# Performance work log

Hardware: AMD Instinct MI355X
Metric: run time of the kernel (lower is better)

## Reference

```python
import jax, jax.numpy as jnp
import numpy as np
from jax import lax

B, A, H, W = 16, 9, 128, 128
STRIDE = 16
MIN_SIZE = 16.0


def _generate_anchors():
    base = 16.0
    ratios = np.array([0.5, 1.0, 2.0])
    scales = np.array([8.0, 16.0, 32.0])
    ctr = (base - 1.0) / 2.0
    size = base * base
    ws0 = np.round(np.sqrt(size / ratios))
    hs0 = np.round(ws0 * ratios)
    ws = (ws0[:, None] * scales[None, :]).reshape(-1)  # [9]
    hs = (hs0[:, None] * scales[None, :]).reshape(-1)
    base_anchors = np.stack([ctr - 0.5 * (ws - 1), ctr - 0.5 * (hs - 1),
                             ctr + 0.5 * (ws - 1), ctr + 0.5 * (hs - 1)], axis=1)  # [9,4]
    sx = np.arange(W) * STRIDE
    sy = np.arange(H) * STRIDE
    shift_x, shift_y = np.meshgrid(sx, sy)  # [H,W]
    shifts = np.stack([shift_x, shift_y, shift_x, shift_y], axis=-1).reshape(H * W, 1, 4)
    return (shifts + base_anchors[None]).reshape(-1, 4).astype(np.float32)  # [H*W*A,4]


def setup_inputs() -> dict:
    key = jax.random.key(0)
    k1, k2 = jax.random.split(key)
    scores = jax.random.normal(k1, (B, 2 * A, H, W), jnp.float32)
    bbox_deltas = jax.random.normal(k2, (B, 4 * A, H, W), jnp.float32) * 0.1
    anchors = jnp.asarray(_generate_anchors())
    im_info = jnp.tile(jnp.array([H * STRIDE, W * STRIDE, 1.0, 1.0], jnp.float32), (B, 1))
    return {"scores": scores, "bbox_deltas": bbox_deltas, "anchors": anchors,
            "im_info": im_info, "num_anchors": A, "pre_nms": 2000, "post_nms": 300,
            "nms_thresh": 0.7}


def _iou_matrix(b):
    x1, y1, x2, y2 = b[:, 0], b[:, 1], b[:, 2], b[:, 3]
    area = (x2 - x1 + 1.0) * (y2 - y1 + 1.0)
    iw = jnp.maximum(jnp.minimum(x2[:, None], x2[None, :]) - jnp.maximum(x1[:, None], x1[None, :]) + 1.0, 0.0)
    ih = jnp.maximum(jnp.minimum(y2[:, None], y2[None, :]) - jnp.maximum(y1[:, None], y1[None, :]) + 1.0, 0.0)
    inter = iw * ih
    return inter / (area[:, None] + area[None, :] - inter)


def reference(scores, bbox_deltas, anchors, im_info, num_anchors, pre_nms, post_nms, nms_thresh):
    batch = bbox_deltas.shape[0]
    feat_w = scores.shape[3]
    # deltas -> [B, H*W*A, 4]
    deltas = bbox_deltas.transpose(0, 2, 3, 1).reshape(batch, -1, 4)
    # fg/bg softmax exactly as in the module
    s = jax.nn.softmax(scores.reshape(batch, 2, -1, feat_w), axis=1)
    s = s.reshape(batch, num_anchors * 2, -1, feat_w)[:, num_anchors:, :, :]
    s = s.transpose(0, 2, 3, 1).reshape(batch, -1)  # [B, H*W*A]
    anc = jnp.broadcast_to(anchors.reshape(1, -1, 4), deltas.shape)
    # bbox_transform_inv
    widths = anc[..., 2] - anc[..., 0] + 1.0
    heights = anc[..., 3] - anc[..., 1] + 1.0
    ctr_x = anc[..., 0] + 0.5 * widths
    ctr_y = anc[..., 1] + 0.5 * heights
    dx, dy, dw, dh = deltas[..., 0], deltas[..., 1], deltas[..., 2], deltas[..., 3]
    pcx = dx * widths + ctr_x
    pcy = dy * heights + ctr_y
    pw = jnp.exp(dw) * widths
    ph = jnp.exp(dh) * heights
    proposals = jnp.stack([pcx - 0.5 * pw, pcy - 0.5 * ph, pcx + 0.5 * pw, pcy + 0.5 * ph], axis=-1)
    # clip_boxes to image extent (im_info = [h, w, sy, sx])
    w_max = (im_info[:, 1] - 1.0)[:, None]
    h_max = (im_info[:, 0] - 1.0)[:, None]
    proposals = jnp.stack([
        jnp.clip(proposals[..., 0], 0.0, w_max),
        jnp.clip(proposals[..., 1], 0.0, h_max),
        jnp.clip(proposals[..., 2], 0.0, w_max),
        jnp.clip(proposals[..., 3], 0.0, h_max)], axis=-1)

    ar = jnp.arange(pre_nms)

    def per_image(props, scr, info):
        ws = props[:, 2] - props[:, 0] + 1.0
        hs = props[:, 3] - props[:, 1] + 1.0
        valid = (ws >= MIN_SIZE * info[3]) & (hs >= MIN_SIZE * info[2])
        masked = jnp.where(valid, scr, -jnp.inf)
        vals, idx = lax.top_k(masked, pre_nms)  # sort desc + truncate to pre_nms
        boxes = props[idx]  # [pre_nms, 4], score-sorted
        live = jnp.isfinite(vals)  # drop filtered boxes if fewer than pre_nms survive
        iou = _iou_matrix(boxes)  # [pre_nms, pre_nms]
        def body(i, keep):
            sup = keep[i] & (iou[i] > nms_thresh) & (ar > i)
            return keep & (~sup)
        keep = lax.fori_loop(0, pre_nms, body, live)  # greedy NMS over sorted boxes
        pos = jnp.where(keep, jnp.cumsum(keep) - 1, post_nms)
        kept = jnp.zeros((post_nms, 4), boxes.dtype).at[pos].set(boxes, mode='drop')
        return kept

    kept = jax.vmap(per_image)(proposals, s, im_info)  # [B, post_nms, 4]
    bidx = jnp.broadcast_to(jnp.arange(batch, dtype=kept.dtype)[:, None, None], (batch, post_nms, 1))
    output = jnp.concatenate([bidx, kept], axis=-1)  # [B, post_nms, 5]
    return output, proposals
```

## Files before the change

kernel.cpp:

```cpp
#include <hip/hip_runtime.h>
#include <stdint.h>

#define B_ 16
#define A_ 9
#define H_ 128
#define W_ 128
#define HW_ (H_*W_)
#define N_ (HW_*A_)
#define PRE_ 2000
#define POST_ 300
#define CAND_CAP 4096
#define SEG_ 32

typedef unsigned int u32;
typedef unsigned long long u64;

#define OFF_STATE  0ull
#define OFF_HIST0  1024ull
#define OFF_HIST1  (OFF_HIST0 + 16384ull)
#define OFF_KEYS   (OFF_HIST1 + 16384ull)
#define OFF_CAND   (OFF_KEYS + (u64)B_*N_*4)
#define OFF_SELBOX (OFF_CAND + (u64)B_*CAND_CAP*8)
#define OFF_LIVE   (OFF_SELBOX + (u64)B_*PRE_*16)
#define OFF_SUPP   (OFF_LIVE + (u64)B_*32*8)

__device__ __forceinline__ u32 mono_key(float f) {
    u32 u = __float_as_uint(f);
    return (u & 0x80000000u) ? ~u : (u | 0x80000000u);
}

__device__ __forceinline__ u64 shfl64(u64 v, int src) {
    u32 lo = (u32)__shfl((int)(u32)(v & 0xFFFFFFFFull), src);
    u32 hi = (u32)__shfl((int)(u32)(v >> 32), src);
    return ((u64)hi << 32) | lo;
}

__device__ __forceinline__ void wave_select256(const u32* __restrict__ hh, u32 need,
                                               u32* __restrict__ out) {
    int lane = threadIdx.x & 63;
    uint4 hv = ((const uint4*)hh)[lane];
    u32 psum = hv.x + hv.y + hv.z + hv.w;
    u32 s = psum;
    #pragma unroll
    for (int off = 1; off < 64; off <<= 1) {
        u32 o = (u32)__shfl_down((int)s, off);
        if (lane + off < 64) s += o;
    }
    u32 S_next = (u32)__shfl_down((int)s, 1);
    if (lane == 63) S_next = 0;
    u32 above[4], cnt[4];
    above[3] = S_next;             cnt[3] = hv.w;
    above[2] = S_next + hv.w;      cnt[2] = hv.z;
    above[1] = above[2] + hv.z;    cnt[1] = hv.y;
    above[0] = above[1] + hv.y;    cnt[0] = hv.x;
    #pragma unroll
    for (int j = 3; j >= 0; --j) {
        if (above[j] < need && above[j] + cnt[j] >= need) {
            out[0] = (u32)(4*lane + j);
            out[1] = need - above[j];
        }
    }
}

__global__ __launch_bounds__(576) void decode_kernel(
        const float* __restrict__ scores,
        const float* __restrict__ deltas,
        const float* __restrict__ anchors,
        const float* __restrict__ im_info,
        float* __restrict__ outprop,
        u32* __restrict__ keys,
        u32* __restrict__ hist0) {
    __shared__ float4 tile[9][65];
    __shared__ float4 sbase[A_];
    __shared__ u32 h[256];
    int tid = threadIdx.x;
    int a = tid >> 6, lane = tid & 63;
    if (tid < A_) sbase[tid] = ((const float4*)anchors)[tid];
    if (tid < 256) h[tid] = 0;
    __syncthreads();

    int b  = blockIdx.x >> 8;
    int pb = blockIdx.x & 255;
    int p0 = pb << 6;
    int p  = p0 + lane;

    float s0 = scores[((b*2*A_ + a)      << 14) + p];
    float s1 = scores[((b*2*A_ + A_ + a) << 14) + p];
    float m  = fmaxf(s0, s1);
    float e0 = expf(s0 - m);
    float e1 = expf(s1 - m);
    float fg = e1 / (e0 + e1);

    float4 base = sbase[a];
    int ix = p & (W_-1), iy = p >> 7;
    float sx = (float)(ix * 16), sy = (float)(iy * 16);
    float ax1 = base.x + sx, ay1 = base.y + sy, ax2 = base.z + sx, ay2 = base.w + sy;

    float w  = ax2 - ax1 + 1.0f;
    float h_ = ay2 - ay1 + 1.0f;
    float cx = ax1 + 0.5f*w;
    float cy = ay1 + 0.5f*h_;

    const float* dbase = deltas + (u64)(((b*4*A_ + 4*a) << 14) + p);
    float dx = dbase[0];
    float dy = dbase[HW_];
    float dw = dbase[2*HW_];
    float dh = dbase[3*HW_];

    float pcx = dx*w  + cx;
    float pcy = dy*h_ + cy;
    float pw  = expf(dw)*w;
    float ph  = expf(dh)*h_;
    float x1 = pcx - 0.5f*pw, y1 = pcy - 0.5f*ph;
    float x2 = pcx + 0.5f*pw, y2 = pcy + 0.5f*ph;

    float wmax = im_info[b*4 + 1] - 1.0f;
    float hmax = im_info[b*4 + 0] - 1.0f;
    x1 = fminf(fmaxf(x1, 0.0f), wmax);
    y1 = fminf(fmaxf(y1, 0.0f), hmax);
    x2 = fminf(fmaxf(x2, 0.0f), wmax);
    y2 = fminf(fmaxf(y2, 0.0f), hmax);

    tile[a][lane] = make_float4(x1, y1, x2, y2);

    float bw = x2 - x1 + 1.0f;
    float bh = y2 - y1 + 1.0f;
    bool valid = (bw >= 16.0f*im_info[b*4 + 3]) && (bh >= 16.0f*im_info[b*4 + 2]);
    float sc = valid ? fg : -__builtin_inff();
    u32 k = mono_key(sc);
    keys[((u64)(b*A_ + a) << 14) + p] = k;
    atomicAdd(&h[k >> 24], 1u);
    __syncthreads();

    int a2 = tid % 9, pl = tid / 9;
    ((float4*)outprop)[(u64)b*N_ + p0*9 + tid] = tile[a2][pl];

    if (tid < 256 && h[tid]) atomicAdd(&hist0[b*256 + tid], h[tid]);
}

__global__ __launch_bounds__(1024) void hist16_kernel(
        const u32* __restrict__ keys, const u32* __restrict__ hist0,
        u32* __restrict__ hist1) {
    int b = blockIdx.x >> 4;
    int slice = blockIdx.x & 15;
    int tid = threadIdx.x;
    __shared__ u32 sel[2];
    __shared__ u32 h[256];
    if (tid < 64) wave_select256(hist0 + b*256, (u32)PRE_, sel);
    for (int i = tid; i < 256; i += 1024) h[i] = 0;
    __syncthreads();
    u32 pfx = sel[0];
    const u32* kb = keys + (u64)b*N_ + slice*(N_/16);
    for (int n = tid; n < N_/16; n += 1024) {
        u32 k = kb[n];
        if ((k >> 24) == pfx) atomicAdd(&h[(k >> 16) & 255u], 1u);
    }
    __syncthreads();
    for (int i = tid; i < 256; i += 1024)
        if (h[i]) atomicAdd(&hist1[b*256 + i], h[i]);
}

__global__ __launch_bounds__(1024) void collect_kernel(
        const u32* __restrict__ keys, const u32* __restrict__ hist0,
        const u32* __restrict__ hist1, u32* __restrict__ state,
        u64* __restrict__ cand) {
    int b = blockIdx.x >> 4;
    int slice = blockIdx.x & 15;
    int tid = threadIdx.x;
    int wave = tid >> 6, lane = tid & 63;
    __shared__ u32 sel8[2], sel16[2];
    __shared__ u32 wbase[16];
    __shared__ u32 s_base;
    if (tid < 64) wave_select256(hist0 + b*256, (u32)PRE_, sel8);
    __syncthreads();
    if (tid < 64) wave_select256(hist1 + b*256, sel8[1], sel16);
    __syncthreads();
    u32 T = (sel8[0] << 24) | (sel16[0] << 16);

    const u32* kb = keys + (u64)b*N_ + slice*(N_/16);
    u64* cb = cand + (u64)b*CAND_CAP;

    u32 kreg[9];
    int c = 0;
    #pragma unroll
    for (int r = 0; r < 9; ++r) {
        kreg[r] = kb[tid + r*1024];
        c += (kreg[r] >= T) ? 1 : 0;
    }

    int x = c;
    #pragma unroll
    for (int off = 1; off < 64; off <<= 1) {
        int y = __shfl_up(x, off);
        if (lane >= off) x += y;
    }
    if (lane == 63) wbase[wave] = (u32)x;
    __syncthreads();
    if (tid == 0) {
        u32 acc = 0;
        #pragma unroll
        for (int w2 = 0; w2 < 16; ++w2) { u32 t2 = wbase[w2]; wbase[w2] = acc; acc += t2; }
        s_base = acc ? atomicAdd(&state[b*8 + 2], acc) : 0u;
    }
    __syncthreads();

    u32 pos = s_base + wbase[wave] + (u32)(x - c);
    #pragma unroll
    for (int r = 0; r < 9; ++r) {
        if (kreg[r] >= T) {
            int idx = slice*(N_/16) + tid + r*1024;
            u32 n = (u32)((idx & (HW_-1))*A_ + (idx >> 14));
            if (pos < CAND_CAP) cb[pos] = ((u64)kreg[r] << 32) | (u32)(~n);
            pos++;
        }
    }
}

__global__ __launch_bounds__(1024) void rank_kernel(
        const u64* __restrict__ cand, const u32* __restrict__ state,
        const float* __restrict__ outprop,
        float4* __restrict__ selbox, u32* __restrict__ selkey) {
    int bi = blockIdx.x;
    int b = bi >> 4, chunk = bi & 15;
    int tid = threadIdx.x;
    int q = tid >> 8, ti = tid & 255;
    __shared__ __align__(16) u64 sc[CAND_CAP];
    __shared__ u32 prank[256];

    u32 cnt = state[b*8 + 2];
    if (cnt > CAND_CAP) cnt = CAND_CAP;
    const u64* cb = cand + (u64)b*CAND_CAP;
    for (int j = tid; j < CAND_CAP; j += 1024) sc[j] = (j < (int)cnt) ? cb[j] : 0ull;
    if (tid < 256) prank[tid] = 0;
    __syncthreads();

    int i = (chunk << 8) + ti;
    u64 mine = sc[i];

    int pairs = ((int)cnt + 1) >> 1;
    int pq = (pairs + 3) >> 2;
    int p0 = q * pq;
    int p1 = p0 + pq; if (p1 > pairs) p1 = pairs;
    const ulonglong2* sl = (const ulonglong2*)sc;
    u32 c = 0;
    #pragma unroll 8
    for (int p = p0; p < p1; ++p) {
        ulonglong2 v = sl[p];
        c += (v.x > mine) ? 1u : 0u;
        c += (v.y > mine) ? 1u : 0u;
    }
    if (c) atomicAdd(&prank[ti], c);
    __syncthreads();

    if (q == 0 && i < (int)cnt) {
        u32 rank = prank[ti];
        if (rank < PRE_) {
            u32 n = ~(u32)mine;
            float4 box = ((const float4*)outprop)[(u64)b*N_ + n];
            selbox[(u64)b*PRE_ + rank] = box;
            selkey[b*2048 + rank] = (u32)(mine >> 32);
        }
    }
}

__global__ __launch_bounds__(256) void iou_kernel(
        const float4* __restrict__ selbox, const float* __restrict__ thrp,
        u64* __restrict__ supp) {
    int bi = blockIdx.x;
    int b = bi / 250;
    int rbase = (bi % 250) * 8;
    int c0 = rbase >> 8;
    int tid = threadIdx.x;
    __shared__ float4 box[PRE_];
    for (int i = (c0 << 8) + tid; i < PRE_; i += 256) box[i] = selbox[(u64)b*PRE_ + i];
    __syncthreads();
    float thresh = thrp[0];
    int wv = tid >> 6, lane = tid & 63;

    float4 p[8]; float ai[8];
    #pragma unroll
    for (int r = 0; r < 8; ++r) {
        p[r]  = box[rbase + r];
        ai[r] = (p[r].z - p[r].x + 1.f) * (p[r].w - p[r].y + 1.f);
    }
    for (int c = c0; c < 8; ++c) {
        int j = c*256 + tid;
        bool inb = (j < PRE_);
        float4 q = box[inb ? j : 0];
        float aj = (q.z - q.x + 1.f) * (q.w - q.y + 1.f);
        #pragma unroll
        for (int r = 0; r < 8; ++r) {
            float iw = fminf(p[r].z, q.z) - fmaxf(p[r].x, q.x) + 1.f;
            float ih = fminf(p[r].w, q.w) - fmaxf(p[r].y, q.y) + 1.f;
            float inter = fmaxf(iw, 0.f) * ih;
            float su = ai[r] + aj;
            float un = su - inter;
            float m  = __fmaf_rn(-thresh, un, inter);
            bool pred = m > 0.0f;
            if (__any(fabsf(m) <= 2.0f)) {
                pred = (inter / un) > thresh;
            }
            pred = pred && inb;
            u64 ball = __ballot(pred);
            if (lane == 0)
                supp[((u64)(b*PRE_ + rbase + r))*32 + (c*4 + wv)] = ball;
        }
    }
}

__global__ __launch_bounds__(256) void scan_kernel(
        const u64* __restrict__ supp, const u32* __restrict__ selkey,
        const float4* __restrict__ selbox, float* __restrict__ out0) {
    int b = blockIdx.x;
    int tid = threadIdx.x;
    int wave = tid >> 6, lane = tid & 63;

    __shared__ u64 sdiag[SEG_][64];
    __shared__ u64 lwords[32];
    __shared__ u64 keptmask[SEG_];
    __shared__ int kept[POST_];
    __shared__ int s_kc;

    for (int e = tid; e < SEG_*64; e += 256) {
        int g = e >> 6;
        sdiag[g][e & 63] = (e < PRE_) ? supp[((u64)(b*PRE_ + e))*32 + g] : 0ull;
    }
    #pragma unroll
    for (int k = 0; k < 8; ++k) {
        int r = k*256 + tid;
        u32 kk = selkey[b*2048 + r];
        u64 bal = __ballot((r < PRE_) && (kk >= 0x80000000u));
        if (lane == 0) lwords[k*4 + wave] = bal;
    }
    if (tid < SEG_) keptmask[tid] = 0ull;
    if (tid == 0) s_kc = 0;
    __syncthreads();

    if (wave == 0) {
        u64 aliveW = (lane < 32) ? lwords[lane] : 0ull;
        int kc = 0;
        for (int g = 0; g < SEG_ && kc < POST_; ++g) {
            u64 aw = shfl64(aliveW, g);
            if (!aw) continue;
            u64 dj = sdiag[g][lane];
            int base = g << 6;

            u64 a = aw;
            u64 ks = 0;
            while (a && kc < POST_) {
                int i = (int)__builtin_ctzll(a);
                ks |= (1ull << i);
                kc++;
                bool killed = ((dj >> i) & 1ull) != 0ull;
                u64 km = __ballot(killed);
                a &= ~km;
                a &= ~(1ull << i);
            }
            if (lane == 0) keptmask[g] = ks;
            if (kc >= POST_) break;

            bool ld = (lane > g) && (lane < 32);
            u64 t = ks;
            u64 orr = 0ull;
            const u64* rb = supp + ((u64)(b*PRE_ + base))*32 + (lane & 31);
            while (t) {
                int i0 = (int)__builtin_ctzll(t);
                int id[16];
                #pragma unroll
                for (int k = 0; k < 16; ++k) {
                    id[k] = t ? (int)__builtin_ctzll(t) : i0;
                    if (t) t &= t - 1;
                }
                u64 v[16];
                #pragma unroll
                for (int k = 0; k < 16; ++k)
                    v[k] = ld ? rb[(u64)id[k] * 32] : 0ull;
                u64 o = 0ull;
                #pragma unroll
                for (int k = 0; k < 16; ++k) o |= v[k];
                orr |= o;
            }
            aliveW &= ~orr;
        }
        if (lane == 0) s_kc = kc;
    }
    __syncthreads();

    if (wave == 0) {
        u64 w = (lane < 32) ? keptmask[lane] : 0ull;
        int pc = (int)__builtin_popcountll(w);
        int x = pc;
        #pragma unroll
        for (int off = 1; off < 64; off <<= 1) {
            int y = __shfl_up(x, off);
            if (lane >= off) x += y;
        }
        int pr = x - pc;
        u64 t = w;
        int c = 0;
        while (t) {
            int bit = (int)__builtin_ctzll(t);
            t &= t - 1;
            int pos = pr + c; c++;
            if (pos < POST_) kept[pos] = lane*64 + bit;
        }
    }
    __syncthreads();

    int kc = s_kc;
    for (int r = tid; r < POST_; r += 256) {
        int i = (r < kc) ? kept[r] : -1;
        float o1 = 0.f, o2 = 0.f, o3 = 0.f, o4 = 0.f;
        if (i >= 0) {
            float4 bx = selbox[(u64)b*PRE_ + i];
            o1 = bx.x; o2 = bx.y; o3 = bx.z; o4 = bx.w;
        }
        float* rowp = out0 + (u64)(b*POST_ + r)*5;
        rowp[0] = (float)b;
        rowp[1] = o1; rowp[2] = o2; rowp[3] = o3; rowp[4] = o4;
    }
}

extern "C" void kernel_launch(void* const* d_in, const int* in_sizes, int n_in,
                              void* d_out, int out_size, void* d_ws, size_t ws_size,
                              hipStream_t stream) {
    const float* scores  = (const float*)d_in[0];
    const float* deltas  = (const float*)d_in[1];
    const float* anchors = (const float*)d_in[2];
    const float* im_info = (const float*)d_in[3];
    const float* thrp    = (const float*)d_in[7];

    float* out0    = (float*)d_out;
    float* outprop = out0 + (u64)B_*POST_*5;

    char* ws = (char*)d_ws;
    u32*    state  = (u32*)   (ws + OFF_STATE);
    u32*    hist0  = (u32*)   (ws + OFF_HIST0);
    u32*    hist1  = (u32*)   (ws + OFF_HIST1);
    u32*    keys   = (u32*)   (ws + OFF_KEYS);
    u64*    cand   = (u64*)   (ws + OFF_CAND);
    float4* selbox = (float4*)(ws + OFF_SELBOX);
    u64*    supp   = (u64*)   (ws + OFF_SUPP);
    u32*    selkey = (u32*)   (ws + OFF_KEYS);

    hipMemsetAsync(ws, 0, OFF_KEYS, stream);

    decode_kernel<<<B_*256, 576, 0, stream>>>(scores, deltas, anchors, im_info, outprop, keys, hist0);
    hist16_kernel<<<B_*16, 1024, 0, stream>>>(keys, hist0, hist1);
    collect_kernel<<<B_*16, 1024, 0, stream>>>(keys, hist0, hist1, state, cand);
    rank_kernel<<<B_*16, 1024, 0, stream>>>(cand, state, outprop, selbox, selkey);
    iou_kernel<<<B_*250, 256, 0, stream>>>(selbox, thrp, supp);
    scan_kernel<<<B_, 256, 0, stream>>>(supp, selkey, selbox, out0);
}
```

Measured before the change: 227.1 us.

## Double-buffer suppression mask segments in shared memory for the NMS scan

The serial NMS scan no longer has wave 0 gather suppression rows from global memory. All four waves now cooperatively prefetch each 64-row segment of the mask matrix into a padded, double-buffered shared-memory tile, working one segment ahead through registers. Wave 0 then reads both the diagonal word and the kept rows from LDS, taking global latency off the serial critical path. The cost is a block-wide barrier per segment, about 34KB of LDS, and extra register pressure from the prefetch staging.

```diff
diff --git a/kernel.cpp b/kernel.cpp
--- a/kernel.cpp
+++ b/kernel.cpp
@@ -308,23 +308,19 @@
     }
 }
 
-__global__ __launch_bounds__(256) void scan_kernel(
+__global__ __launch_bounds__(256, 1) void scan_kernel(
         const u64* __restrict__ supp, const u32* __restrict__ selkey,
         const float4* __restrict__ selbox, float* __restrict__ out0) {
     int b = blockIdx.x;
     int tid = threadIdx.x;
     int wave = tid >> 6, lane = tid & 63;
 
-    __shared__ u64 sdiag[SEG_][64];
+    __shared__ u64 rbuf[2][64][33];
     __shared__ u64 lwords[32];
     __shared__ u64 keptmask[SEG_];
     __shared__ int kept[POST_];
     __shared__ int s_kc;
 
-    for (int e = tid; e < SEG_*64; e += 256) {
-        int g = e >> 6;
-        sdiag[g][e & 63] = (e < PRE_) ? supp[((u64)(b*PRE_ + e))*32 + g] : 0ull;
-    }
     #pragma unroll
     for (int k = 0; k < 8; ++k) {
         int r = k*256 + tid;
@@ -334,57 +330,90 @@
     }
     if (tid < SEG_) keptmask[tid] = 0ull;
     if (tid == 0) s_kc = 0;
-    __syncthreads();
-
-    if (wave == 0) {
-        u64 aliveW = (lane < 32) ? lwords[lane] : 0ull;
-        int kc = 0;
-        for (int g = 0; g < SEG_ && kc < POST_; ++g) {
+
+    const u64* sb = supp + (u64)b*PRE_*32;
+
+    u64 gr[8];
+    #pragma unroll
+    for (int k = 0; k < 8; ++k) {
+        int f = tid + (k << 8);
+        gr[k] = sb[(u64)(f >> 5)*32 + (f & 31)];
+    }
+    #pragma unroll
+    for (int k = 0; k < 8; ++k) {
+        int f = tid + (k << 8);
+        rbuf[0][f >> 5][f & 31] = gr[k];
+    }
+    #pragma unroll
+    for (int k = 0; k < 8; ++k) {
+        int f = tid + (k << 8);
+        gr[k] = sb[(u64)(64 + (f >> 5))*32 + (f & 31)];
+    }
+    __syncthreads();
+
+    u64 aliveW = 0ull;
+    if (wave == 0 && lane < 32) aliveW = lwords[lane];
+    int kc = 0;
+    int ll = lane & 31;
+
+    for (int g = 0; g < SEG_; ++g) {
+        int cur = g & 1;
+        if (g + 1 < SEG_) {
+            #pragma unroll
+            for (int k = 0; k < 8; ++k) {
+                int f = tid + (k << 8);
+                rbuf[cur ^ 1][f >> 5][f & 31] = gr[k];
+            }
+        }
+        if (g + 2 < SEG_) {
+            #pragma unroll
+            for (int k = 0; k < 8; ++k) {
+                int f = tid + (k << 8);
+                int row = ((g + 2) << 6) + (f >> 5);
+                if (row > PRE_ - 1) row = PRE_ - 1;
+                gr[k] = sb[(u64)row*32 + (f & 31)];
+            }
+        }
+        if (wave == 0) {
             u64 aw = shfl64(aliveW, g);
-            if (!aw) continue;
-            u64 dj = sdiag[g][lane];
-            int base = g << 6;
-
-            u64 a = aw;
-            u64 ks = 0;
-            while (a && kc < POST_) {
-                int i = (int)__builtin_ctzll(a);
-                ks |= (1ull << i);
-                kc++;
-                bool killed = ((dj >> i) & 1ull) != 0ull;
-                u64 km = __ballot(killed);
-                a &= ~km;
-                a &= ~(1ull << i);
+            if (aw) {
+                u64 dj = rbuf[cur][lane][g];
+                u64 a = aw, ks = 0ull;
+                while (a && kc < POST_) {
+                    int i = (int)__builtin_ctzll(a);
+                    ks |= (1ull << i);
+                    kc++;
+                    bool killed = ((dj >> i) & 1ull) != 0ull;
+                    u64 km = __ballot(killed);
+                    a &= ~km;
+                    a &= ~(1ull << i);
+                }
+                if (lane == 0) keptmask[g] = ks;
+                if (kc < POST_) {
+                    u64 t = ks, orr = 0ull;
+                    while (t) {
+                        int i0 = (int)__builtin_ctzll(t);
+                        #define GJ(n) int j##n = t ? (int)__builtin_ctzll(t) : i0; if (t) t &= t - 1;
+                        GJ(0) GJ(1) GJ(2) GJ(3) GJ(4) GJ(5) GJ(6) GJ(7)
+                        #undef GJ
+                        u64 r0 = rbuf[cur][j0][ll];
+                        u64 r1 = rbuf[cur][j1][ll];
+                        u64 r2 = rbuf[cur][j2][ll];
+                        u64 r3 = rbuf[cur][j3][ll];
+                        u64 r4 = rbuf[cur][j4][ll];
+                        u64 r5 = rbuf[cur][j5][ll];
+                        u64 r6 = rbuf[cur][j6][ll];
+                        u64 r7 = rbuf[cur][j7][ll];
+                        orr |= ((r0 | r1) | (r2 | r3)) | ((r4 | r5) | (r6 | r7));
+                    }
+                    aliveW &= ~orr;
+                }
             }
-            if (lane == 0) keptmask[g] = ks;
-            if (kc >= POST_) break;
-
-            bool ld = (lane > g) && (lane < 32);
-            u64 t = ks;
-            u64 orr = 0ull;
-            const u64* rb = supp + ((u64)(b*PRE_ + base))*32 + (lane & 31);
-            while (t) {
-                int i0 = (int)__builtin_ctzll(t);
-                int id[16];
-                #pragma unroll
-                for (int k = 0; k < 16; ++k) {
-                    id[k] = t ? (int)__builtin_ctzll(t) : i0;
-                    if (t) t &= t - 1;
-                }
-                u64 v[16];
-                #pragma unroll
-                for (int k = 0; k < 16; ++k)
-                    v[k] = ld ? rb[(u64)id[k] * 32] : 0ull;
-                u64 o = 0ull;
-                #pragma unroll
-                for (int k = 0; k < 16; ++k) o |= v[k];
-                orr |= o;
-            }
-            aliveW &= ~orr;
-        }
-        if (lane == 0) s_kc = kc;
-    }
-    __syncthreads();
+            if (lane == 0) s_kc = kc;
+        }
+        __syncthreads();
+        if (s_kc >= POST_) break;
+    }
 
     if (wave == 0) {
         u64 w = (lane < 32) ? keptmask[lane] : 0ull;
@@ -407,9 +436,9 @@
     }
     __syncthreads();
 
-    int kc = s_kc;
+    int kc2 = s_kc;
     for (int r = tid; r < POST_; r += 256) {
-        int i = (r < kc) ? kept[r] : -1;
+        int i = (r < kc2) ? kept[r] : -1;
         float o1 = 0.f, o2 = 0.f, o3 = 0.f, o4 = 0.f;
         if (i >= 0) {
             float4 bx = selbox[(u64)b*PRE_ + i];
```

Result: faster. 222.5 us (-2.0%).
